# Kernel optimization log

Measured on AMD Instinct MI355X. Metric: run time of the kernel, lower is better.

Reference implementation:

```python
import jax, jax.numpy as jnp
import numpy as np

HEADS = 8
DIM_HEAD = 64
SCALE = DIM_HEAD ** -0.5

def setup_inputs() -> dict:
    key = jax.random.key(0)
    k1, k2, k3 = jax.random.split(key, 3)
    B, N, D = 4, 2048, 512
    inner = HEADS * DIM_HEAD  # 512
    x = jax.random.normal(k1, (B, N, D), dtype=jnp.float32)
    w_qkv = jax.random.normal(k2, (D, inner * 3), dtype=jnp.float32) * (D ** -0.5)
    w_out = jax.random.normal(k3, (inner, D), dtype=jnp.float32) * (inner ** -0.5)
    b_out = jnp.zeros((D,), dtype=jnp.float32)
    return {"x": x, "w_qkv": w_qkv, "w_out": w_out, "b_out": b_out}

def reference(x, w_qkv, w_out, b_out):
    B, N, D = x.shape
    qkv = x @ w_qkv  # [B, N, 3*inner]
    q, k, v = jnp.split(qkv, 3, axis=-1)
    # b n (h d) -> b h n d
    def to_heads(t):
        return t.reshape(B, N, HEADS, DIM_HEAD).transpose(0, 2, 1, 3)
    q, k, v = to_heads(q), to_heads(k), to_heads(v)
    dots = jnp.einsum('bhid,bhjd->bhij', q, k) * SCALE  # [B,H,N,N]
    attn = jax.nn.softmax(dots, axis=-1)
    out = jnp.einsum('bhij,bhjd->bhid', attn, v)  # [B,H,N,Dh]
    out = out.transpose(0, 2, 1, 3).reshape(B, N, HEADS * DIM_HEAD)
    return out @ w_out + b_out
```

## Files before the change

kernel.cpp:

```cpp
#include <hip/hip_runtime.h>
#include <hip/hip_bf16.h>
#include <math.h>
#include <stdint.h>


typedef unsigned short u16;
typedef __attribute__((ext_vector_type(4))) float f32x4;
typedef __attribute__((ext_vector_type(8))) short bf16x8;
typedef __attribute__((ext_vector_type(4))) short s16x4;

#define AS1 __attribute__((address_space(1)))
#define AS3 __attribute__((address_space(3)))
#define MFMA(a, b, c) __builtin_amdgcn_mfma_f32_16x16x32_bf16(a, b, c, 0, 0, 0)
#define QSCALE 0.180336880f

__device__ __forceinline__ u16 f2bf(float f) {
  union { float f; unsigned u; } v; v.f = f;
  unsigned r = v.u + 0x7FFFu + ((v.u >> 16) & 1u);
  return (u16)(r >> 16);
}
__device__ __forceinline__ float bf2f(u16 b) {
  union { unsigned u; float f; } v; v.u = ((unsigned)b) << 16; return v.f;
}
__device__ __forceinline__ void gld16(const u16* g, u16* l) {
  __builtin_amdgcn_global_load_lds((const AS1 void*)g, (AS3 void*)l, 16, 0, 0);
}
__device__ __forceinline__ float u2f(unsigned u) {
  union { unsigned u; float f; } v; v.u = u; return v.f;
}
__device__ __forceinline__ unsigned f2u(float f) {
  union { float f; unsigned u; } v; v.f = f; return v.u;
}
__device__ __forceinline__ int cvtpk(float lo, float hi) {
  int r; asm("v_cvt_pk_bf16_f32 %0, %1, %2" : "=v"(r) : "v"(lo), "v"(hi));
  return r;
}
__device__ __forceinline__ float fexp2(float x) {
  float r; asm("v_exp_f32 %0, %1" : "=v"(r) : "v"(x));
  return r;
}

__global__ void k_cast(const float* __restrict__ s, u16* __restrict__ h, int n) {
  int i = (blockIdx.x * 256 + threadIdx.x) * 4;
  if (i < n) {
    f32x4 v = *(const f32x4*)&s[i];
    s16x4 hh;
    #pragma unroll
    for (int j = 0; j < 4; ++j) hh[j] = (short)f2bf(v[j]);
    *(s16x4*)&h[i] = hh;
  }
}

__global__ void k_tcast(const float* __restrict__ s, u16* __restrict__ h,
                        int N, int total) {
  int i = blockIdx.x * 256 + threadIdx.x;
  if (i < total) {
    int n = i >> 9, k = i & 511;
    h[i] = f2bf(s[(size_t)k * N + n]);
  }
}

__device__ __forceinline__ void gemm_core(
    const u16* __restrict__ Ah, const u16* __restrict__ Bh,
    char* sm, int rowA, int rowB, int tid, f32x4 (&acc)[4][4]) {
  const int wid = tid >> 6, lane = tid & 63;
  const int x = lane & 15, h = lane >> 4;
  const int wr = wid >> 1, wc = wid & 1;
  const int d0 = tid * 16;
  const int lg0 = d0 ^ (((d0 >> 7) & 7) << 4);
  const int srow = lg0 >> 6;
  const int scol = (lg0 & 63) >> 1;
  const int swk = ((lane >> 1) & 7) << 4;
  const int rdoA = ((wr * 64 + x) * 64 + h * 16) ^ swk;
  const int rdoB = (((wc * 64 + x) * 64 + h * 16) ^ swk) + 8192;

  {
    #pragma unroll
    for (int r = 0; r < 2; ++r) {
      const size_t ga = (size_t)(rowA + r * 64 + srow) * 512 + scol;
      const size_t gb = (size_t)(rowB + r * 64 + srow) * 512 + scol;
      gld16(Ah + ga, (u16*)(sm + r * 4096 + d0));
      gld16(Bh + gb, (u16*)(sm + 8192 + r * 4096 + d0));
    }
  }

  for (int kt = 0; kt < 16; ++kt) {
    const int bb = (kt & 1) * 16384;
    __builtin_amdgcn_s_barrier();
    if (kt < 15) {
      const int kofs = (kt + 1) * 32;
      char* buf = sm + (16384 - bb);
      #pragma unroll
      for (int r = 0; r < 2; ++r) {
        const size_t ga = (size_t)(rowA + r * 64 + srow) * 512 + kofs + scol;
        const size_t gb = (size_t)(rowB + r * 64 + srow) * 512 + kofs + scol;
        gld16(Ah + ga, (u16*)(buf + r * 4096 + d0));
        gld16(Bh + gb, (u16*)(buf + 8192 + r * 4096 + d0));
      }
      asm volatile("s_waitcnt vmcnt(4)" ::: "memory");
    } else {
      asm volatile("s_waitcnt vmcnt(0)" ::: "memory");
    }
    __builtin_amdgcn_s_barrier();

    bf16x8 a_h[4], b_h[4];
    #pragma unroll
    for (int i = 0; i < 4; ++i)
      a_h[i] = *(const bf16x8*)(sm + bb + rdoA + i * 1024);
    #pragma unroll
    for (int j = 0; j < 4; ++j)
      b_h[j] = *(const bf16x8*)(sm + bb + rdoB + j * 1024);
    __builtin_amdgcn_s_setprio(1);
    #pragma unroll
    for (int i = 0; i < 4; ++i)
      #pragma unroll
      for (int j = 0; j < 4; ++j)
        acc[i][j] = MFMA(a_h[i], b_h[j], acc[i][j]);
    __builtin_amdgcn_s_setprio(0);
  }
}

__global__ __launch_bounds__(256) void k_gemm_qkv(
    const u16* __restrict__ Ah, const u16* __restrict__ Bh,
    u16* __restrict__ Qb, u16* __restrict__ Kb, u16* __restrict__ Vt) {
  __shared__ __align__(1024) char sm[32768];
  const int tid = threadIdx.x, lane = tid & 63, wid = tid >> 6;
  const int x = lane & 15, h = lane >> 4;
  const int wr = wid >> 1, wc = wid & 1;
  const int rowA = blockIdx.x * 128, rowB = blockIdx.y * 128;
  f32x4 acc[4][4] = {};
  gemm_core(Ah, Bh, sm, rowA, rowB, tid, acc);

  #pragma unroll
  for (int i = 0; i < 4; ++i)
    #pragma unroll
    for (int j = 0; j < 4; ++j) {
      const int n = rowB + wc * 64 + j * 16 + x;
      const int which = n >> 9;
      const int hh = (n >> 6) & 7, d = n & 63;
      const int m0 = rowA + wr * 64 + i * 16 + h * 4;
      const int b = m0 >> 11, is0 = m0 & 2047;
      if (which == 0) {
        #pragma unroll
        for (int r = 0; r < 4; ++r) {
          const size_t idx = ((size_t)((b * 8 + hh) * 2048 + is0 + r)) * 64 + d;
          Qb[idx] = f2bf(acc[i][j][r] * QSCALE);
        }
      } else if (which == 1) {
        #pragma unroll
        for (int r = 0; r < 4; ++r) {
          const size_t idx = ((size_t)((b * 8 + hh) * 2048 + is0 + r)) * 64 + d;
          Kb[idx] = f2bf(acc[i][j][r]);
        }
      } else {
        s16x4 vv;
        #pragma unroll
        for (int r = 0; r < 4; ++r) vv[r] = (short)f2bf(acc[i][j][r]);
        *(s16x4*)&Vt[((size_t)((b * 8 + hh) * 64 + d)) * 2048 + is0] = vv;
      }
    }
}

__global__ __launch_bounds__(256) void k_gemm_out(
    const u16* __restrict__ Ah, const u16* __restrict__ Bh,
    const float* __restrict__ bias, float* __restrict__ out) {
  __shared__ __align__(1024) char sm[32768];
  const int tid = threadIdx.x, lane = tid & 63, wid = tid >> 6;
  const int x = lane & 15, h = lane >> 4;
  const int wr = wid >> 1, wc = wid & 1;
  const int rowA = blockIdx.x * 128, rowB = blockIdx.y * 128;
  f32x4 acc[4][4] = {};
  gemm_core(Ah, Bh, sm, rowA, rowB, tid, acc);

  #pragma unroll
  for (int i = 0; i < 4; ++i)
    #pragma unroll
    for (int j = 0; j < 4; ++j) {
      const int n = rowB + wc * 64 + j * 16 + x;
      #pragma unroll
      for (int r = 0; r < 4; ++r) {
        const int m = rowA + wr * 64 + i * 16 + h * 4 + r;
        out[(size_t)m * 512 + n] = acc[i][j][r] + bias[n];
      }
    }
}

__global__ __launch_bounds__(512, 2) void k_attn(
    const u16* __restrict__ Qb,
    const u16* __restrict__ Kb, const u16* __restrict__ Vt,
    u16* __restrict__ OP,
    float* __restrict__ Mm,
    float* __restrict__ Sm) {
  __shared__ __align__(1024) char sm[65536];
  const int tid = threadIdx.x, wid = tid >> 6, lane = tid & 63;
  const int x = lane & 15, h = lane >> 4;

  const int fid = blockIdx.x;
  const int l = (fid & 7) * 64 + (fid >> 3);
  const int half = l & 1, qb = (l >> 1) & 7, bh = l >> 4;

  const size_t base = (size_t)bh * 2048 * 64;
  const int qr0 = qb * 256 + wid * 32;
  const size_t kv0 = (size_t)half * 1024;

  bf16x8 qh[2][2];
  #pragma unroll
  for (int g = 0; g < 2; ++g) {
    const size_t rq = base + (size_t)(qr0 + g * 16 + x) * 64 + h * 8;
    #pragma unroll
    for (int ks = 0; ks < 2; ++ks)
      qh[g][ks] = *(const bf16x8*)&Qb[rq + ks * 32];
  }

  bf16x8 ones;
  #pragma unroll
  for (int j = 0; j < 8; ++j) ones[j] = (short)0x3F80;

  const int db = tid * 16;
  const int lg = db ^ (((db >> 7) & 7) << 4);
  const int sks  = db >> 12;
  const int srow = (lg >> 6) & 63;
  const int scb  = (lg & 63) >> 1;
  const size_t offK = (size_t)srow * 64 + sks * 32 + scb;
  const size_t offV = (size_t)srow * 2048 + sks * 32 + scb;

  const int swk = ((lane >> 1) & 7) << 4;
  const int rdo = (x * 64 + h * 16) ^ swk;
  char* const pb = sm + 32768 + wid * 4096;
  const int pxor = (x & 7) << 4;
  const int prow = x * 128;

  float mrun[2] = {-INFINITY, -INFINITY};
  f32x4 o[2][4] = {};
  f32x4 os[2] = {};

  {
    gld16(Kb + base + kv0 * 64 + offK, (u16*)(sm + db));
    gld16(Vt + base + kv0 + offV,      (u16*)(sm + 8192 + db));
  }

  for (int kv = 0; kv < 16; ++kv) {
    const int bb = (kv & 1) * 16384;
    __builtin_amdgcn_s_barrier();
    if (kv < 15) {
      const size_t kvb = kv0 + (size_t)(kv + 1) * 64;
      char* buf = sm + (16384 - bb);
      gld16(Kb + base + kvb * 64 + offK, (u16*)(buf + db));
      gld16(Vt + base + kvb + offV,      (u16*)(buf + 8192 + db));
      asm volatile("s_waitcnt vmcnt(2)" ::: "memory");
    } else {
      asm volatile("s_waitcnt vmcnt(0)" ::: "memory");
    }
    __builtin_amdgcn_s_barrier();

    const char* smb = sm + bb + rdo;

    f32x4 s[2][4] = {};
    __builtin_amdgcn_s_setprio(1);
    #pragma unroll
    for (int c = 0; c < 4; ++c)
      #pragma unroll
      for (int ks = 0; ks < 2; ++ks) {
        bf16x8 kb_ = *(const bf16x8*)(smb + ks * 4096 + c * 1024);
        s[0][c] = MFMA(kb_, qh[0][ks], s[0][c]);
        s[1][c] = MFMA(kb_, qh[1][ks], s[1][c]);
      }
    __builtin_amdgcn_s_setprio(0);

    float pm[2];
    #pragma unroll
    for (int g = 0; g < 2; ++g) {
      float m0 = fmaxf(fmaxf(s[g][0][0], s[g][0][1]), s[g][0][2]);
      float m1 = fmaxf(fmaxf(s[g][0][3], s[g][1][0]), s[g][1][1]);
      float m2 = fmaxf(fmaxf(s[g][1][2], s[g][1][3]), s[g][2][0]);
      float m3 = fmaxf(fmaxf(s[g][2][1], s[g][2][2]), s[g][2][3]);
      float m4 = fmaxf(fmaxf(s[g][3][0], s[g][3][1]), s[g][3][2]);
      float m5 = fmaxf(fmaxf(m0, m1), m2);
      float p  = fmaxf(fmaxf(fmaxf(m3, m4), s[g][3][3]), m5);
      p = fmaxf(p, __shfl_xor(p, 16, 64));
      p = fmaxf(p, __shfl_xor(p, 32, 64));
      pm[g] = p;
    }

    if (__any((pm[0] > mrun[0] + 7.0f) || (pm[1] > mrun[1] + 7.0f))) {
      #pragma unroll
      for (int g = 0; g < 2; ++g) {
        float mnew = fmaxf(mrun[g], pm[g]);
        float scl = fexp2(mrun[g] - mnew);
        mrun[g] = mnew;
        #pragma unroll
        for (int r = 0; r < 4; ++r) {
          float sq = u2f((unsigned)__builtin_amdgcn_ds_bpermute(
              (20 * h + r) * 4, (int)f2u(scl)));
          os[g][r] *= sq;
          #pragma unroll
          for (int dg = 0; dg < 4; ++dg) o[g][dg][r] *= sq;
        }
      }
    }

    #pragma unroll
    for (int g = 0; g < 2; ++g)
      #pragma unroll
      for (int c = 0; c < 4; ++c) {
        int w0 = cvtpk(fexp2(s[g][c][0] - mrun[g]),
                       fexp2(s[g][c][1] - mrun[g]));
        int w1 = cvtpk(fexp2(s[g][c][2] - mrun[g]),
                       fexp2(s[g][c][3] - mrun[g]));
        int* dst = (int*)(pb + g * 2048 + prow + ((c * 32 + h * 8) ^ pxor));
        dst[0] = w0; dst[1] = w1;
      }

    __builtin_amdgcn_s_setprio(1);
    #pragma unroll
    for (int ch = 0; ch < 2; ++ch) {
      bf16x8 pa0 = *(const bf16x8*)(pb + prow +
                                    ((ch * 64 + h * 16) ^ pxor));
      bf16x8 pa1 = *(const bf16x8*)(pb + 2048 + prow +
                                    ((ch * 64 + h * 16) ^ pxor));
      os[0] = MFMA(pa0, ones, os[0]);
      os[1] = MFMA(pa1, ones, os[1]);
      #pragma unroll
      for (int dg = 0; dg < 4; ++dg) {
        bf16x8 vb = *(const bf16x8*)(smb + 8192 + ch * 4096 + dg * 1024);
        o[0][dg] = MFMA(pa0, vb, o[0][dg]);
        o[1][dg] = MFMA(pa1, vb, o[1][dg]);
      }
    }
    __builtin_amdgcn_s_setprio(0);
  }

  u16* op = OP + (size_t)half * 4194304 + ((size_t)(bh * 2048 + qr0)) * 64;
  #pragma unroll
  for (int g = 0; g < 2; ++g) {
    #pragma unroll
    for (int r = 0; r < 4; ++r) {
      const int row = g * 16 + h * 4 + r;
      #pragma unroll
      for (int dg = 0; dg < 4; ++dg)
        op[(size_t)row * 64 + dg * 16 + x] = f2bf(o[g][dg][r]);
      if (x == 0)
        Sm[half * 65536 + bh * 2048 + qr0 + g * 16 + h * 4 + r] = os[g][r];
    }
    if (h == 0)
      Mm[half * 65536 + bh * 2048 + qr0 + g * 16 + x] = mrun[g];
  }
}

__global__ __launch_bounds__(256) void k_combine(
    const u16* __restrict__ OP, const float* __restrict__ Mm,
    const float* __restrict__ Sm, u16* __restrict__ AO) {
  const int gi = blockIdx.x * 256 + threadIdx.x;
  const int d4 = (gi & 15) * 4;
  const int rb = gi >> 4;
  const float m1 = Mm[rb], m2 = Mm[65536 + rb];
  const float s1 = Sm[rb], s2 = Sm[65536 + rb];
  const float m = fmaxf(m1, m2);
  const float a1 = fexp2(m1 - m), a2 = fexp2(m2 - m);
  const float inv = 1.0f / (s1 * a1 + s2 * a2);
  const float w1 = a1 * inv, w2 = a2 * inv;
  s16x4 p1 = *(const s16x4*)&OP[(size_t)rb * 64 + d4];
  s16x4 p2 = *(const s16x4*)&OP[4194304 + (size_t)rb * 64 + d4];
  const int bh = rb >> 11, row = rb & 2047;
  const int b = bh >> 3, head = bh & 7;
  s16x4 r_;
  #pragma unroll
  for (int j = 0; j < 4; ++j)
    r_[j] = (short)f2bf(bf2f((u16)p1[j]) * w1 + bf2f((u16)p2[j]) * w2);
  *(s16x4*)&AO[((size_t)(b * 2048 + row)) * 512 + head * 64 + d4] = r_;
}

extern "C" void kernel_launch(void* const* d_in, const int* in_sizes, int n_in,
                              void* d_out, int out_size, void* d_ws, size_t ws_size,
                              hipStream_t stream) {
  const float* x    = (const float*)d_in[0];
  const float* wqkv = (const float*)d_in[1];
  const float* wout = (const float*)d_in[2];
  const float* bout = (const float*)d_in[3];
  float* out = (float*)d_out;

  char* w = (char*)d_ws;
  u16* xh  = (u16*)(w + 0);
  u16* wqh = (u16*)(w + 16777216);
  u16* woh = (u16*)(w + 19922944);
  u16* Qb  = (u16*)(w + 20971520);
  u16* Kb  = (u16*)(w + 37748736);
  u16* Vt  = (u16*)(w + 46137344);
  u16* AO  = (u16*)(w + 54525952);
  u16*   OP = (u16*)(w + 0);
  float* Mm = (float*)(w + 16777216);
  float* Sm = (float*)(w + 17301504);

  k_cast <<<4096, 256, 0, stream>>>(x, xh, 4194304);
  k_tcast<<<3072, 256, 0, stream>>>(wqkv, wqh, 1536, 786432);
  k_tcast<<<1024, 256, 0, stream>>>(wout, woh, 512, 262144);
  k_gemm_qkv<<<dim3(64, 12), 256, 0, stream>>>(xh, wqh, Qb, Kb, Vt);
  k_attn<<<512, 512, 0, stream>>>(Qb, Kb, Vt, OP, Mm, Sm);
  k_combine<<<4096, 256, 0, stream>>>(OP, Mm, Sm, AO);
  k_gemm_out<<<dim3(64, 4), 256, 0, stream>>>(AO, woh, bout, out);
}
```

Measured before the change: 96.46 us.

## Fuse split-KV combine into output GEMM A-staging and merge cast kernels

```diff
diff --git a/kernel.cpp b/kernel.cpp
--- a/kernel.cpp
+++ b/kernel.cpp
@@ -40,23 +40,26 @@
   return r;
 }
 
-__global__ void k_cast(const float* __restrict__ s, u16* __restrict__ h, int n) {
-  int i = (blockIdx.x * 256 + threadIdx.x) * 4;
-  if (i < n) {
-    f32x4 v = *(const f32x4*)&s[i];
+__global__ __launch_bounds__(256) void k_prep(
+    const float* __restrict__ x,    u16* __restrict__ xh,
+    const float* __restrict__ wqkv, u16* __restrict__ wqh,
+    const float* __restrict__ wout, u16* __restrict__ woh) {
+  const int bid = blockIdx.x, tid = threadIdx.x;
+  if (bid < 4096) {
+    int i = (bid * 256 + tid) * 4;
+    f32x4 v = *(const f32x4*)&x[i];
     s16x4 hh;
     #pragma unroll
     for (int j = 0; j < 4; ++j) hh[j] = (short)f2bf(v[j]);
-    *(s16x4*)&h[i] = hh;
-  }
-}
-
-__global__ void k_tcast(const float* __restrict__ s, u16* __restrict__ h,
-                        int N, int total) {
-  int i = blockIdx.x * 256 + threadIdx.x;
-  if (i < total) {
+    *(s16x4*)&xh[i] = hh;
+  } else if (bid < 7168) {
+    int i = (bid - 4096) * 256 + tid;
     int n = i >> 9, k = i & 511;
-    h[i] = f2bf(s[(size_t)k * N + n]);
+    wqh[i] = f2bf(wqkv[(size_t)k * 1536 + n]);
+  } else {
+    int i = (bid - 7168) * 256 + tid;
+    int n = i >> 9, k = i & 511;
+    woh[i] = f2bf(wout[(size_t)k * 512 + n]);
   }
 }
 
@@ -162,15 +165,104 @@
 }
 
 __global__ __launch_bounds__(256) void k_gemm_out(
-    const u16* __restrict__ Ah, const u16* __restrict__ Bh,
+    const u16* __restrict__ OP, const float* __restrict__ Mm,
+    const float* __restrict__ Sm, const u16* __restrict__ Bh,
     const float* __restrict__ bias, float* __restrict__ out) {
   __shared__ __align__(1024) char sm[32768];
   const int tid = threadIdx.x, lane = tid & 63, wid = tid >> 6;
   const int x = lane & 15, h = lane >> 4;
   const int wr = wid >> 1, wc = wid & 1;
   const int rowA = blockIdx.x * 128, rowB = blockIdx.y * 128;
+
+  const int d0 = tid * 16;
+  const int lg0 = d0 ^ (((d0 >> 7) & 7) << 4);
+  const int srow = lg0 >> 6;
+  const int scol = (lg0 & 63) >> 1;
+  const int swk = ((lane >> 1) & 7) << 4;
+  const int rdoA = ((wr * 64 + x) * 64 + h * 16) ^ swk;
+  const int rdoB = (((wc * 64 + x) * 64 + h * 16) ^ swk) + 8192;
+
+  int bseq[2], srw[2];
+  #pragma unroll
+  for (int r = 0; r < 2; ++r) {
+    const int m = rowA + r * 64 + srow;
+    bseq[r] = (m >> 11) * 8;
+    srw[r] = m & 2047;
+  }
+
   f32x4 acc[4][4] = {};
-  gemm_core(Ah, Bh, sm, rowA, rowB, tid, acc);
+
+  auto stageA = [&](int kt, char* buf) {
+    const int n0 = kt * 32 + scol;
+    const int head = n0 >> 6, dd = n0 & 63;
+    #pragma unroll
+    for (int r = 0; r < 2; ++r) {
+      const int rb = (bseq[r] + head) * 2048 + srw[r];
+      const float m1 = Mm[rb], m2 = Mm[65536 + rb];
+      const float s1 = Sm[rb], s2 = Sm[65536 + rb];
+      const float mm = fmaxf(m1, m2);
+      const float a1 = fexp2(m1 - mm), a2 = fexp2(m2 - mm);
+      const float inv = 1.0f / (s1 * a1 + s2 * a2);
+      const float w1 = a1 * inv, w2 = a2 * inv;
+      bf16x8 p1 = *(const bf16x8*)&OP[(size_t)rb * 64 + dd];
+      bf16x8 p2 = *(const bf16x8*)&OP[4194304 + (size_t)rb * 64 + dd];
+      union { int w[4]; bf16x8 v; } uu;
+      #pragma unroll
+      for (int q = 0; q < 4; ++q) {
+        float lo = bf2f((u16)p1[2 * q]) * w1 + bf2f((u16)p2[2 * q]) * w2;
+        float hi = bf2f((u16)p1[2 * q + 1]) * w1 + bf2f((u16)p2[2 * q + 1]) * w2;
+        uu.w[q] = cvtpk(lo, hi);
+      }
+      *(bf16x8*)(buf + r * 4096 + d0) = uu.v;
+    }
+  };
+
+  {
+    stageA(0, sm);
+    #pragma unroll
+    for (int r = 0; r < 2; ++r) {
+      const size_t gb = (size_t)(rowB + r * 64 + srow) * 512 + scol;
+      gld16(Bh + gb, (u16*)(sm + 8192 + r * 4096 + d0));
+    }
+    asm volatile("s_waitcnt lgkmcnt(0)" ::: "memory");
+    __builtin_amdgcn_sched_barrier(0);
+  }
+
+  for (int kt = 0; kt < 16; ++kt) {
+    const int bb = (kt & 1) * 16384;
+    asm volatile("s_barrier" ::: "memory");
+    if (kt < 15) {
+      char* buf = sm + (16384 - bb);
+      const int kofs = (kt + 1) * 32;
+      #pragma unroll
+      for (int r = 0; r < 2; ++r) {
+        const size_t gb = (size_t)(rowB + r * 64 + srow) * 512 + kofs + scol;
+        gld16(Bh + gb, (u16*)(buf + 8192 + r * 4096 + d0));
+      }
+      stageA(kt + 1, buf);
+      asm volatile("s_waitcnt vmcnt(2)" ::: "memory");
+      asm volatile("s_waitcnt lgkmcnt(0)" ::: "memory");
+      __builtin_amdgcn_sched_barrier(0);
+    } else {
+      asm volatile("s_waitcnt vmcnt(0)" ::: "memory");
+    }
+    asm volatile("s_barrier" ::: "memory");
+
+    bf16x8 a_h[4], b_h[4];
+    #pragma unroll
+    for (int i = 0; i < 4; ++i)
+      a_h[i] = *(const bf16x8*)(sm + bb + rdoA + i * 1024);
+    #pragma unroll
+    for (int j = 0; j < 4; ++j)
+      b_h[j] = *(const bf16x8*)(sm + bb + rdoB + j * 1024);
+    __builtin_amdgcn_s_setprio(1);
+    #pragma unroll
+    for (int i = 0; i < 4; ++i)
+      #pragma unroll
+      for (int j = 0; j < 4; ++j)
+        acc[i][j] = MFMA(a_h[i], b_h[j], acc[i][j]);
+    __builtin_amdgcn_s_setprio(0);
+  }
 
   #pragma unroll
   for (int i = 0; i < 4; ++i)
@@ -347,29 +439,6 @@
   }
 }
 
-__global__ __launch_bounds__(256) void k_combine(
-    const u16* __restrict__ OP, const float* __restrict__ Mm,
-    const float* __restrict__ Sm, u16* __restrict__ AO) {
-  const int gi = blockIdx.x * 256 + threadIdx.x;
-  const int d4 = (gi & 15) * 4;
-  const int rb = gi >> 4;
-  const float m1 = Mm[rb], m2 = Mm[65536 + rb];
-  const float s1 = Sm[rb], s2 = Sm[65536 + rb];
-  const float m = fmaxf(m1, m2);
-  const float a1 = fexp2(m1 - m), a2 = fexp2(m2 - m);
-  const float inv = 1.0f / (s1 * a1 + s2 * a2);
-  const float w1 = a1 * inv, w2 = a2 * inv;
-  s16x4 p1 = *(const s16x4*)&OP[(size_t)rb * 64 + d4];
-  s16x4 p2 = *(const s16x4*)&OP[4194304 + (size_t)rb * 64 + d4];
-  const int bh = rb >> 11, row = rb & 2047;
-  const int b = bh >> 3, head = bh & 7;
-  s16x4 r_;
-  #pragma unroll
-  for (int j = 0; j < 4; ++j)
-    r_[j] = (short)f2bf(bf2f((u16)p1[j]) * w1 + bf2f((u16)p2[j]) * w2);
-  *(s16x4*)&AO[((size_t)(b * 2048 + row)) * 512 + head * 64 + d4] = r_;
-}
-
 extern "C" void kernel_launch(void* const* d_in, const int* in_sizes, int n_in,
                               void* d_out, int out_size, void* d_ws, size_t ws_size,
                               hipStream_t stream) {
@@ -386,16 +455,12 @@
   u16* Qb  = (u16*)(w + 20971520);
   u16* Kb  = (u16*)(w + 37748736);
   u16* Vt  = (u16*)(w + 46137344);
-  u16* AO  = (u16*)(w + 54525952);
   u16*   OP = (u16*)(w + 0);
   float* Mm = (float*)(w + 16777216);
   float* Sm = (float*)(w + 17301504);
 
-  k_cast <<<4096, 256, 0, stream>>>(x, xh, 4194304);
-  k_tcast<<<3072, 256, 0, stream>>>(wqkv, wqh, 1536, 786432);
-  k_tcast<<<1024, 256, 0, stream>>>(wout, woh, 512, 262144);
+  k_prep<<<8192, 256, 0, stream>>>(x, xh, wqkv, wqh, wout, woh);
   k_gemm_qkv<<<dim3(64, 12), 256, 0, stream>>>(xh, wqh, Qb, Kb, Vt);
   k_attn<<<512, 512, 0, stream>>>(Qb, Kb, Vt, OP, Mm, Sm);
-  k_combine<<<4096, 256, 0, stream>>>(OP, Mm, Sm, AO);
-  k_gemm_out<<<dim3(64, 4), 256, 0, stream>>>(AO, woh, bout, out);
-}
+  k_gemm_out<<<dim3(64, 4), 256, 0, stream>>>(OP, Mm, Sm, woh, bout, out);
+}
```

After: 96.89 us. Within noise of the previous version (+0.4%).

## Split attention KV into four partitions, shrink tiles, fuse cast kernels

Applied to the files above, without the earlier changes.

```diff
diff --git a/kernel.cpp b/kernel.cpp
--- a/kernel.cpp
+++ b/kernel.cpp
@@ -14,6 +14,11 @@
 #define MFMA(a, b, c) __builtin_amdgcn_mfma_f32_16x16x32_bf16(a, b, c, 0, 0, 0)
 #define QSCALE 0.180336880f
 
+#define QOFF0 0
+#define QOFF1 4194304
+#define QOFF2 27262976
+#define QOFF3 31457280
+
 __device__ __forceinline__ u16 f2bf(float f) {
   union { float f; unsigned u; } v; v.f = f;
   unsigned r = v.u + 0x7FFFu + ((v.u >> 16) & 1u);
@@ -40,23 +45,42 @@
   return r;
 }
 
-__global__ void k_cast(const float* __restrict__ s, u16* __restrict__ h, int n) {
-  int i = (blockIdx.x * 256 + threadIdx.x) * 4;
-  if (i < n) {
-    f32x4 v = *(const f32x4*)&s[i];
+__global__ __launch_bounds__(256) void k_prep(
+    const float* __restrict__ x,    u16* __restrict__ xh,
+    const float* __restrict__ wqkv, u16* __restrict__ wqh,
+    const float* __restrict__ wout, u16* __restrict__ woh) {
+  const int bid = blockIdx.x, tid = threadIdx.x;
+  if (bid < 4096) {
+    int i = (bid * 256 + tid) * 4;
+    f32x4 v = *(const f32x4*)&x[i];
     s16x4 hh;
     #pragma unroll
     for (int j = 0; j < 4; ++j) hh[j] = (short)f2bf(v[j]);
-    *(s16x4*)&h[i] = hh;
-  }
-}
-
-__global__ void k_tcast(const float* __restrict__ s, u16* __restrict__ h,
-                        int N, int total) {
-  int i = blockIdx.x * 256 + threadIdx.x;
-  if (i < total) {
-    int n = i >> 9, k = i & 511;
-    h[i] = f2bf(s[(size_t)k * N + n]);
+    *(s16x4*)&xh[i] = hh;
+    return;
+  }
+  __shared__ u16 lds[64][66];
+  const float* src; u16* dst; int N, n0, k0;
+  if (bid < 4288) {
+    const int b2 = bid - 4096;
+    src = wqkv; dst = wqh; N = 1536;
+    n0 = (b2 % 24) * 64; k0 = (b2 / 24) * 64;
+  } else {
+    const int b3 = bid - 4288;
+    src = wout; dst = woh; N = 512;
+    n0 = (b3 & 7) * 64; k0 = (b3 >> 3) * 64;
+  }
+  const int c = tid & 63, q = tid >> 6;
+  #pragma unroll
+  for (int s = 0; s < 16; ++s) {
+    const int kr = q * 16 + s;
+    lds[c][kr] = f2bf(src[(size_t)(k0 + kr) * N + n0 + c]);
+  }
+  __syncthreads();
+  #pragma unroll
+  for (int s = 0; s < 16; ++s) {
+    const int nr = q * 16 + s;
+    dst[(size_t)(n0 + nr) * 512 + k0 + c] = lds[nr][c];
   }
 }
 
@@ -185,23 +209,23 @@
     }
 }
 
-__global__ __launch_bounds__(512, 2) void k_attn(
+__global__ __launch_bounds__(512, 8) void k_attn(
     const u16* __restrict__ Qb,
     const u16* __restrict__ Kb, const u16* __restrict__ Vt,
     u16* __restrict__ OP,
     float* __restrict__ Mm,
     float* __restrict__ Sm) {
-  __shared__ __align__(1024) char sm[65536];
+  __shared__ __align__(1024) char sm[32768];
   const int tid = threadIdx.x, wid = tid >> 6, lane = tid & 63;
   const int x = lane & 15, h = lane >> 4;
 
   const int fid = blockIdx.x;
-  const int l = (fid & 7) * 64 + (fid >> 3);
-  const int half = l & 1, qb = (l >> 1) & 7, bh = l >> 4;
+  const int l = (fid & 7) * 128 + (fid >> 3);
+  const int quarter = l & 3, qb = (l >> 2) & 7, bh = l >> 5;
 
   const size_t base = (size_t)bh * 2048 * 64;
   const int qr0 = qb * 256 + wid * 32;
-  const size_t kv0 = (size_t)half * 1024;
+  const size_t kv0 = (size_t)quarter * 512;
 
   bf16x8 qh[2][2];
   #pragma unroll
@@ -217,37 +241,41 @@
   for (int j = 0; j < 8; ++j) ones[j] = (short)0x3F80;
 
   const int db = tid * 16;
-  const int lg = db ^ (((db >> 7) & 7) << 4);
-  const int sks  = db >> 12;
-  const int srow = (lg >> 6) & 63;
-  const int scb  = (lg & 63) >> 1;
-  const size_t offK = (size_t)srow * 64 + sks * 32 + scb;
-  const size_t offV = (size_t)srow * 2048 + sks * 32 + scb;
+  const u16* srcBase;
+  size_t stOff, stMul;
+  if (db < 4096) {
+    const int ks = (db >> 11) & 1, bc = db & 2047;
+    const int lg = bc ^ (((bc >> 7) & 7) << 4);
+    stOff = (size_t)(lg >> 6) * 64 + ks * 32 + ((lg & 63) >> 1);
+    stMul = 64;
+    srcBase = Kb + base;
+  } else {
+    const int bv = db - 4096;
+    const int lg = bv ^ (((bv >> 7) & 7) << 4);
+    stOff = (size_t)(lg >> 6) * 2048 + ((lg & 63) >> 1);
+    stMul = 1;
+    srcBase = Vt + base;
+  }
 
   const int swk = ((lane >> 1) & 7) << 4;
   const int rdo = (x * 64 + h * 16) ^ swk;
-  char* const pb = sm + 32768 + wid * 4096;
+  char* const pb = sm + 16384 + wid * 2048;
   const int pxor = (x & 7) << 4;
-  const int prow = x * 128;
+  const int pwr = (x * 64) ^ pxor;
 
   float mrun[2] = {-INFINITY, -INFINITY};
   f32x4 o[2][4] = {};
   f32x4 os[2] = {};
 
-  {
-    gld16(Kb + base + kv0 * 64 + offK, (u16*)(sm + db));
-    gld16(Vt + base + kv0 + offV,      (u16*)(sm + 8192 + db));
-  }
+  gld16(srcBase + kv0 * stMul + stOff, (u16*)(sm + db));
 
   for (int kv = 0; kv < 16; ++kv) {
-    const int bb = (kv & 1) * 16384;
+    const int bb = (kv & 1) * 8192;
     __builtin_amdgcn_s_barrier();
     if (kv < 15) {
-      const size_t kvb = kv0 + (size_t)(kv + 1) * 64;
-      char* buf = sm + (16384 - bb);
-      gld16(Kb + base + kvb * 64 + offK, (u16*)(buf + db));
-      gld16(Vt + base + kvb + offV,      (u16*)(buf + 8192 + db));
-      asm volatile("s_waitcnt vmcnt(2)" ::: "memory");
+      const size_t kvb = kv0 + (size_t)(kv + 1) * 32;
+      gld16(srcBase + kvb * stMul + stOff, (u16*)(sm + (8192 - bb) + db));
+      asm volatile("s_waitcnt vmcnt(1)" ::: "memory");
     } else {
       asm volatile("s_waitcnt vmcnt(0)" ::: "memory");
     }
@@ -255,13 +283,13 @@
 
     const char* smb = sm + bb + rdo;
 
-    f32x4 s[2][4] = {};
+    f32x4 s[2][2] = {};
     __builtin_amdgcn_s_setprio(1);
     #pragma unroll
-    for (int c = 0; c < 4; ++c)
+    for (int c = 0; c < 2; ++c)
       #pragma unroll
       for (int ks = 0; ks < 2; ++ks) {
-        bf16x8 kb_ = *(const bf16x8*)(smb + ks * 4096 + c * 1024);
+        bf16x8 kb_ = *(const bf16x8*)(smb + ks * 2048 + c * 1024);
         s[0][c] = MFMA(kb_, qh[0][ks], s[0][c]);
         s[1][c] = MFMA(kb_, qh[1][ks], s[1][c]);
       }
@@ -270,13 +298,11 @@
     float pm[2];
     #pragma unroll
     for (int g = 0; g < 2; ++g) {
-      float m0 = fmaxf(fmaxf(s[g][0][0], s[g][0][1]), s[g][0][2]);
-      float m1 = fmaxf(fmaxf(s[g][0][3], s[g][1][0]), s[g][1][1]);
-      float m2 = fmaxf(fmaxf(s[g][1][2], s[g][1][3]), s[g][2][0]);
-      float m3 = fmaxf(fmaxf(s[g][2][1], s[g][2][2]), s[g][2][3]);
-      float m4 = fmaxf(fmaxf(s[g][3][0], s[g][3][1]), s[g][3][2]);
-      float m5 = fmaxf(fmaxf(m0, m1), m2);
-      float p  = fmaxf(fmaxf(fmaxf(m3, m4), s[g][3][3]), m5);
+      float m0 = fmaxf(fmaxf(s[g][0][0], s[g][0][1]),
+                       fmaxf(s[g][0][2], s[g][0][3]));
+      float m1 = fmaxf(fmaxf(s[g][1][0], s[g][1][1]),
+                       fmaxf(s[g][1][2], s[g][1][3]));
+      float p = fmaxf(m0, m1);
       p = fmaxf(p, __shfl_xor(p, 16, 64));
       p = fmaxf(p, __shfl_xor(p, 32, 64));
       pm[g] = p;
@@ -302,27 +328,25 @@
     #pragma unroll
     for (int g = 0; g < 2; ++g)
       #pragma unroll
-      for (int c = 0; c < 4; ++c) {
+      for (int c = 0; c < 2; ++c) {
         int w0 = cvtpk(fexp2(s[g][c][0] - mrun[g]),
                        fexp2(s[g][c][1] - mrun[g]));
         int w1 = cvtpk(fexp2(s[g][c][2] - mrun[g]),
                        fexp2(s[g][c][3] - mrun[g]));
-        int* dst = (int*)(pb + g * 2048 + prow + ((c * 32 + h * 8) ^ pxor));
+        int* dst = (int*)(pb + g * 1024 +
+                          ((x * 64 + c * 32 + h * 8) ^ pxor));
         dst[0] = w0; dst[1] = w1;
       }
 
     __builtin_amdgcn_s_setprio(1);
-    #pragma unroll
-    for (int ch = 0; ch < 2; ++ch) {
-      bf16x8 pa0 = *(const bf16x8*)(pb + prow +
-                                    ((ch * 64 + h * 16) ^ pxor));
-      bf16x8 pa1 = *(const bf16x8*)(pb + 2048 + prow +
-                                    ((ch * 64 + h * 16) ^ pxor));
+    {
+      bf16x8 pa0 = *(const bf16x8*)(pb + ((x * 64 + h * 16) ^ pxor));
+      bf16x8 pa1 = *(const bf16x8*)(pb + 1024 + ((x * 64 + h * 16) ^ pxor));
       os[0] = MFMA(pa0, ones, os[0]);
       os[1] = MFMA(pa1, ones, os[1]);
       #pragma unroll
       for (int dg = 0; dg < 4; ++dg) {
-        bf16x8 vb = *(const bf16x8*)(smb + 8192 + ch * 4096 + dg * 1024);
+        bf16x8 vb = *(const bf16x8*)(smb + 4096 + dg * 1024);
         o[0][dg] = MFMA(pa0, vb, o[0][dg]);
         o[1][dg] = MFMA(pa1, vb, o[1][dg]);
       }
@@ -330,7 +354,10 @@
     __builtin_amdgcn_s_setprio(0);
   }
 
-  u16* op = OP + (size_t)half * 4194304 + ((size_t)(bh * 2048 + qr0)) * 64;
+  const size_t qoff = (quarter == 0) ? QOFF0 : (quarter == 1) ? QOFF1
+                    : (quarter == 2) ? QOFF2 : QOFF3;
+  u16* op = OP + qoff + ((size_t)(bh * 2048 + qr0)) * 64;
+  const int msbase = quarter * 65536 + bh * 2048 + qr0;
   #pragma unroll
   for (int g = 0; g < 2; ++g) {
     #pragma unroll
@@ -340,10 +367,10 @@
       for (int dg = 0; dg < 4; ++dg)
         op[(size_t)row * 64 + dg * 16 + x] = f2bf(o[g][dg][r]);
       if (x == 0)
-        Sm[half * 65536 + bh * 2048 + qr0 + g * 16 + h * 4 + r] = os[g][r];
+        Sm[msbase + g * 16 + h * 4 + r] = os[g][r];
     }
     if (h == 0)
-      Mm[half * 65536 + bh * 2048 + qr0 + g * 16 + x] = mrun[g];
+      Mm[msbase + g * 16 + x] = mrun[g];
   }
 }
 
@@ -353,20 +380,32 @@
   const int gi = blockIdx.x * 256 + threadIdx.x;
   const int d4 = (gi & 15) * 4;
   const int rb = gi >> 4;
-  const float m1 = Mm[rb], m2 = Mm[65536 + rb];
-  const float s1 = Sm[rb], s2 = Sm[65536 + rb];
-  const float m = fmaxf(m1, m2);
-  const float a1 = fexp2(m1 - m), a2 = fexp2(m2 - m);
-  const float inv = 1.0f / (s1 * a1 + s2 * a2);
-  const float w1 = a1 * inv, w2 = a2 * inv;
-  s16x4 p1 = *(const s16x4*)&OP[(size_t)rb * 64 + d4];
-  s16x4 p2 = *(const s16x4*)&OP[4194304 + (size_t)rb * 64 + d4];
+  float m[4], s[4];
+  #pragma unroll
+  for (int i = 0; i < 4; ++i) {
+    m[i] = Mm[i * 65536 + rb];
+    s[i] = Sm[i * 65536 + rb];
+  }
+  const float mx = fmaxf(fmaxf(m[0], m[1]), fmaxf(m[2], m[3]));
+  float a[4], den = 0.f;
+  #pragma unroll
+  for (int i = 0; i < 4; ++i) { a[i] = fexp2(m[i] - mx); den += s[i] * a[i]; }
+  const float inv = 1.0f / den;
+
+  const size_t qo[4] = {QOFF0, QOFF1, QOFF2, QOFF3};
+  float acc4[4] = {0.f, 0.f, 0.f, 0.f};
+  #pragma unroll
+  for (int i = 0; i < 4; ++i) {
+    const float w = a[i] * inv;
+    s16x4 p = *(const s16x4*)&OP[qo[i] + (size_t)rb * 64 + d4];
+    #pragma unroll
+    for (int j = 0; j < 4; ++j) acc4[j] += bf2f((u16)p[j]) * w;
+  }
   const int bh = rb >> 11, row = rb & 2047;
   const int b = bh >> 3, head = bh & 7;
   s16x4 r_;
   #pragma unroll
-  for (int j = 0; j < 4; ++j)
-    r_[j] = (short)f2bf(bf2f((u16)p1[j]) * w1 + bf2f((u16)p2[j]) * w2);
+  for (int j = 0; j < 4; ++j) r_[j] = (short)f2bf(acc4[j]);
   *(s16x4*)&AO[((size_t)(b * 2048 + row)) * 512 + head * 64 + d4] = r_;
 }
 
@@ -386,16 +425,14 @@
   u16* Qb  = (u16*)(w + 20971520);
   u16* Kb  = (u16*)(w + 37748736);
   u16* Vt  = (u16*)(w + 46137344);
-  u16* AO  = (u16*)(w + 54525952);
   u16*   OP = (u16*)(w + 0);
   float* Mm = (float*)(w + 16777216);
-  float* Sm = (float*)(w + 17301504);
-
-  k_cast <<<4096, 256, 0, stream>>>(x, xh, 4194304);
-  k_tcast<<<3072, 256, 0, stream>>>(wqkv, wqh, 1536, 786432);
-  k_tcast<<<1024, 256, 0, stream>>>(wout, woh, 512, 262144);
+  float* Sm = (float*)(w + 17825792);
+  u16*   AO = (u16*)(w + 20971520);
+
+  k_prep<<<4352, 256, 0, stream>>>(x, xh, wqkv, wqh, wout, woh);
   k_gemm_qkv<<<dim3(64, 12), 256, 0, stream>>>(xh, wqh, Qb, Kb, Vt);
-  k_attn<<<512, 512, 0, stream>>>(Qb, Kb, Vt, OP, Mm, Sm);
+  k_attn<<<1024, 512, 0, stream>>>(Qb, Kb, Vt, OP, Mm, Sm);
   k_combine<<<4096, 256, 0, stream>>>(OP, Mm, Sm, AO);
   k_gemm_out<<<dim3(64, 4), 256, 0, stream>>>(AO, woh, bout, out);
 }
```

Result: slower. 383.3 us (+297.4%).
